# Kernel optimization log

Hardware: AMD Instinct MI355X
Metric: run time of the kernel (lower is better)

Reference implementation:

```python
import jax, jax.numpy as jnp
import numpy as np

HEADS = 4
DIM_HEAD = 32


def setup_inputs() -> dict:
    key = jax.random.key(0)
    k1, k2, k3, k4 = jax.random.split(key, 4)
    dim = 64
    hidden = HEADS * DIM_HEAD  # 128
    x = jax.random.normal(k1, (2, dim, 48, 48, 48), dtype=jnp.float32)
    # 1x1x1 Conv3d weights are just channel-mixing matrices
    w_qkv = jax.random.normal(k2, (3 * hidden, dim), dtype=jnp.float32) * (1.0 / np.sqrt(dim))
    w_out = jax.random.normal(k3, (dim, hidden), dtype=jnp.float32) * (1.0 / np.sqrt(hidden))
    b_out = jax.random.normal(k4, (dim,), dtype=jnp.float32) * 0.01
    return {"x": x, "w_qkv": w_qkv, "w_out": w_out, "b_out": b_out}


def reference(x, w_qkv, w_out, b_out):
    b, c, X, Y, Z = x.shape
    N = X * Y * Z
    xf = x.reshape(b, c, N)  # flatten spatial dims
    # to_qkv: 1x1x1 conv == channel matmul -> [b, 3*H*C, N]
    qkv = jnp.einsum('bci,oc->boi', xf, w_qkv)
    qkv = qkv.reshape(b, 3, HEADS, DIM_HEAD, N)
    q, k, v = qkv[:, 0], qkv[:, 1], qkv[:, 2]  # each [b, h, c, N]
    q = jax.nn.softmax(q, axis=-2)  # softmax over channel dim
    k = jax.nn.softmax(k, axis=-1)  # softmax over spatial dim
    # linear attention: small [c, d] context per head, O(N)
    ctx = jnp.einsum('bhci,bhdi->bhcd', k, v)   # [b, h, c, d]
    out = jnp.einsum('bhcd,bhck->bhdk', ctx, q)  # [b, h, d, N]
    out = out.reshape(b, HEADS * DIM_HEAD, N)
    # combine_heads: 1x1x1 conv with bias
    out = jnp.einsum('bci,oc->boi', out, w_out) + b_out[None, :, None]
    return out.reshape(b, -1, X, Y, Z)
```

## Files before the change

kernel.cpp:

```cpp
#include <hip/hip_runtime.h>
#include <hip/hip_bf16.h>

typedef unsigned int u32;
typedef unsigned short u16;
typedef __attribute__((ext_vector_type(8))) short bf16x8;
typedef __attribute__((ext_vector_type(4))) float f32x4;

#define NPIX 110592
#define NTILES 1728
#define K1_BLOCKS 864
#define K1_TPB 4
#define PART_STRIDE 4224

#define WS_ATB   0
#define WS_P2    8192
#define WS_XPK   75776
#define WS_PART  7153664

union FragU { u32 u[4]; bf16x8 v; };

#define MFMA(a,b,c) __builtin_amdgcn_mfma_f32_16x16x32_bf16((a),(b),(c),0,0,0)

__device__ __forceinline__ void gll16(const float* g, float* l) {
    typedef const __attribute__((address_space(1))) unsigned int* gp_t;
    typedef __attribute__((address_space(3))) unsigned int* lp_t;
    __builtin_amdgcn_global_load_lds((gp_t)g, (lp_t)l, 16, 0, 0);
}
__device__ __forceinline__ u32 pk2(float a, float b) {
    union { __hip_bfloat162 h2; u32 u; } cv;
    cv.h2.x = __float2bfloat16(a);
    cv.h2.y = __float2bfloat16(b);
    return cv.u;
}

__global__ __launch_bounds__(256, 3)
void k1_ctx(const float* __restrict__ x, const float* __restrict__ wq,
            float* __restrict__ ws, int usePart, int R) {
    __shared__ u32 xbh[256 * 32];
    const int blk = blockIdx.x;
    const int p   = threadIdx.x & 63;
    const int og  = __builtin_amdgcn_readfirstlane(threadIdx.x >> 6);
    const int b   = blk / (K1_BLOCKS / 2);
    const int q   = p >> 4;
    const int l15 = p & 15;
    const int yv  = (p & 7) << 2;
    const float* xg = x + (long)b * 64 * NPIX;
    float* part = ws + WS_PART;

    FragU wh[4][2];
    #pragma unroll
    for (int mi = 0; mi < 4; ++mi)
        #pragma unroll
        for (int ks = 0; ks < 2; ++ks) {
            const int kvrow = (mi < 2) ? (og * 32 + mi * 16) : (128 + og * 32 + (mi - 2) * 16);
            const int row = 128 + kvrow + l15;
            const float* wp = wq + row * 64 + ks * 32 + q * 4;
            float4 f0 = *(const float4*)wp;
            float4 f1 = *(const float4*)(wp + 16);
            wh[mi][ks].u[0] = pk2(f0.x, f0.y);
            wh[mi][ks].u[1] = pk2(f0.z, f0.w);
            wh[mi][ks].u[2] = pk2(f1.x, f1.y);
            wh[mi][ks].u[3] = pk2(f1.z, f1.w);
        }

    FragU ones;
    #pragma unroll
    for (int i = 0; i < 4; ++i) ones.u[i] = 0x3F803F80u;

    f32x4 cc[2][2], rsa[2];
    #pragma unroll
    for (int mi = 0; mi < 2; ++mi) {
        #pragma unroll
        for (int ni = 0; ni < 2; ++ni) cc[mi][ni] = (f32x4)0.f;
        rsa[mi] = (f32x4)0.f;
    }

    const long i0g = (long)(blk * K1_TPB - b * NTILES) * 64;
    #pragma unroll
    for (int ch = 0; ch < 2; ++ch) {
        f32x4 xl4[8];
        const float* xr = xg + (long)(og * 16 + ch * 8) * NPIX + i0g + 4 * p;
        #pragma unroll
        for (int i = 0; i < 8; ++i) xl4[i] = *(const f32x4*)(xr + (long)i * NPIX);
        #pragma unroll
        for (int j = 0; j < 4; ++j) {
            const int px = 4 * p + j;
            const int yy = (px & 7) << 2;
            u32 h[4];
            #pragma unroll
            for (int w = 0; w < 4; ++w) h[w] = pk2(xl4[2 * w][j], xl4[2 * w + 1][j]);
            const int sA = (og * 8 + ch * 4) ^ yy;
            *(uint4*)&xbh[px * 32 + sA] = make_uint4(h[0], h[1], h[2], h[3]);
        }
    }
    __syncthreads();

    {
        u32* xpk = (u32*)ws + WS_XPK + (long)blk * 8192;
        #pragma unroll
        for (int i = 0; i < 8; ++i) {
            const int idx = i * 1024 + threadIdx.x * 4;
            uint4 v = *(const uint4*)&xbh[idx];
            *(uint4*)&xpk[idx] = v;
        }
    }

    #pragma unroll 1
    for (int tt = 0; tt < K1_TPB; ++tt) {
        #pragma unroll
        for (int ksp = 0; ksp < 2; ++ksp) {
            f32x4 acc[4][2];
            #pragma unroll
            for (int ni2 = 0; ni2 < 2; ++ni2) {
                const int ni = ksp * 2 + ni2;
                const int rb = (tt * 64 + ni * 16 + l15) * 32;
                FragU bh[2];
                #pragma unroll
                for (int ks = 0; ks < 2; ++ks) {
                    const int c0 = (ks * 16 + 2 * q) ^ yv;
                    const int c1 = (ks * 16 + 2 * q + 8) ^ yv;
                    uint2 t0 = *(const uint2*)&xbh[rb + c0];
                    uint2 t1 = *(const uint2*)&xbh[rb + c1];
                    bh[ks].u[0] = t0.x; bh[ks].u[1] = t0.y;
                    bh[ks].u[2] = t1.x; bh[ks].u[3] = t1.y;
                }
                #pragma unroll
                for (int mi = 0; mi < 4; ++mi) {
                    f32x4 a = (f32x4)0.f;
                    #pragma unroll
                    for (int ks = 0; ks < 2; ++ks)
                        a = MFMA(bh[ks].v, wh[mi][ks].v, a);
                    acc[mi][ni2] = a;
                }
            }
            FragU ak[2], av[2];
            #pragma unroll
            for (int m2 = 0; m2 < 2; ++m2) {
                float e0[4], e1[4];
                #pragma unroll
                for (int j = 0; j < 4; ++j) {
                    e0[j] = __expf(acc[m2][0][j]);
                    e1[j] = __expf(acc[m2][1][j]);
                }
                ak[m2].u[0] = pk2(e0[0], e0[1]);
                ak[m2].u[1] = pk2(e0[2], e0[3]);
                ak[m2].u[2] = pk2(e1[0], e1[1]);
                ak[m2].u[3] = pk2(e1[2], e1[3]);
                av[m2].u[0] = pk2(acc[2 + m2][0][0], acc[2 + m2][0][1]);
                av[m2].u[1] = pk2(acc[2 + m2][0][2], acc[2 + m2][0][3]);
                av[m2].u[2] = pk2(acc[2 + m2][1][0], acc[2 + m2][1][1]);
                av[m2].u[3] = pk2(acc[2 + m2][1][2], acc[2 + m2][1][3]);
            }
            #pragma unroll
            for (int mi = 0; mi < 2; ++mi) {
                #pragma unroll
                for (int nj = 0; nj < 2; ++nj)
                    cc[mi][nj] = MFMA(ak[mi].v, av[nj].v, cc[mi][nj]);
                rsa[mi] = MFMA(ak[mi].v, ones.v, rsa[mi]);
            }
        }
    }

    if (usePart) {
        float* pp = part + (long)blk * PART_STRIDE;
        #pragma unroll
        for (int mi = 0; mi < 2; ++mi)
            #pragma unroll
            for (int ni = 0; ni < 2; ++ni)
                #pragma unroll
                for (int j = 0; j < 4; ++j)
                    pp[og * 1024 + (mi * 16 + q * 4 + j) * 32 + ni * 16 + l15] = cc[mi][ni][j];
        if (l15 == 0) {
            #pragma unroll
            for (int mi = 0; mi < 2; ++mi)
                #pragma unroll
                for (int j = 0; j < 4; ++j)
                    pp[4096 + og * 32 + mi * 16 + q * 4 + j] = rsa[mi][j];
        }
    } else {
        float* pp = part + (long)(b * R + (blk % R)) * PART_STRIDE;
        #pragma unroll
        for (int mi = 0; mi < 2; ++mi)
            #pragma unroll
            for (int ni = 0; ni < 2; ++ni)
                #pragma unroll
                for (int j = 0; j < 4; ++j)
                    atomicAdd(&pp[og * 1024 + (mi * 16 + q * 4 + j) * 32 + ni * 16 + l15], cc[mi][ni][j]);
        if (l15 == 0) {
            #pragma unroll
            for (int mi = 0; mi < 2; ++mi)
                #pragma unroll
                for (int j = 0; j < 4; ++j)
                    atomicAdd(&pp[4096 + og * 32 + mi * 16 + q * 4 + j], rsa[mi][j]);
        }
    }
}

__global__ __launch_bounds__(128)
void k1b_reduce(float* __restrict__ ws, int PB) {
    const int S = 8;
    const int chunk = blockIdx.x % 33;
    const int rem   = blockIdx.x / 33;
    const int b     = rem & 1;
    const int slice = rem >> 1;
    const int j = chunk * 128 + threadIdx.x;
    const int PBh = PB >> 1;
    const float* part = ws + WS_PART;
    float s = 0.f;
    for (int pi = b * PBh + slice; pi < (b + 1) * PBh; pi += S)
        s += part[(long)pi * PART_STRIDE + j];
    ws[WS_P2 + (long)(b * S + slice) * PART_STRIDE + j] = s;
}

__global__ __launch_bounds__(256)
void k2_prepA(const float* __restrict__ wout, float* __restrict__ ws) {
    __shared__ float wo[64 * 129];
    __shared__ float ct[4096];
    __shared__ float rsum[128];
    const int b   = blockIdx.x >> 3;
    const int jb  = blockIdx.x & 7;
    const int tid = threadIdx.x;
    for (int i = tid; i < 8192; i += 256) wo[(i >> 7) * 129 + (i & 127)] = wout[i];
    for (int i = tid; i < 4096; i += 256) {
        float s = 0.f;
        #pragma unroll
        for (int s8 = 0; s8 < 8; ++s8)
            s += ws[WS_P2 + (long)(b * 8 + s8) * PART_STRIDE + i];
        ct[i] = s;
    }
    if (tid < 128) {
        float s = 0.f;
        #pragma unroll
        for (int s8 = 0; s8 < 8; ++s8)
            s += ws[WS_P2 + (long)(b * 8 + s8) * PART_STRIDE + 4096 + tid];
        rsum[tid] = s;
    }
    __syncthreads();
    u32* atb = (u32*)ws + WS_ATB + b * 4096;
    const int o  = tid & 63;
    const int ug = tid >> 6;
    #pragma unroll
    for (int i = 0; i < 2; ++i) {
        const int up = jb * 8 + ug * 2 + i;
        const int hc0 = 2 * up, hc1 = 2 * up + 1;
        const int hh = hc0 >> 5;
        const int c0 = hc0 & 31, c1 = hc1 & 31;
        float s0 = 0.f, s1 = 0.f;
        #pragma unroll
        for (int d = 0; d < 32; ++d) {
            const float w = wo[o * 129 + hh * 32 + d];
            s0 = fmaf(w, ct[hh * 1024 + c0 * 32 + d], s0);
            s1 = fmaf(w, ct[hh * 1024 + c1 * 32 + d], s1);
        }
        atb[up * 64 + o] = pk2(s0 / rsum[hc0], s1 / rsum[hc1]);
    }
}

__global__ __launch_bounds__(256, 3)
void k3_out(const float* __restrict__ x, const float* __restrict__ wq,
            const float* __restrict__ bout, const float* __restrict__ wsf,
            float* __restrict__ out) {
    __shared__ u32 xbh[256 * 32];
    __shared__ u16 qb[64 * 128];
    const int blk = blockIdx.x;
    const int p   = threadIdx.x & 63;
    const int og  = __builtin_amdgcn_readfirstlane(threadIdx.x >> 6);
    const int b   = blk / (K1_BLOCKS / 2);
    const int q   = p >> 4;
    const int l15 = p & 15;
    const int yv  = (p & 7) << 2;
    (void)x;

    {
        const u32* xpk = (const u32*)wsf + WS_XPK + (long)blk * 8192;
        #pragma unroll
        for (int i = 0; i < 8; ++i) {
            const int o32 = og * 2048 + i * 256;
            gll16((const float*)&xpk[o32 + 4 * p], (float*)&xbh[o32]);
        }
    }

    FragU wh[2][2];
    #pragma unroll
    for (int mi = 0; mi < 2; ++mi)
        #pragma unroll
        for (int ks = 0; ks < 2; ++ks) {
            const int row = og * 32 + mi * 16 + l15;
            const float* wp = wq + row * 64 + ks * 32 + q * 4;
            float4 f0 = *(const float4*)wp;
            float4 f1 = *(const float4*)(wp + 16);
            wh[mi][ks].u[0] = pk2(f0.x, f0.y);
            wh[mi][ks].u[1] = pk2(f0.z, f0.w);
            wh[mi][ks].u[2] = pk2(f1.x, f1.y);
            wh[mi][ks].u[3] = pk2(f1.z, f1.w);
        }

    const u32* atb = (const u32*)wsf + WS_ATB + b * 4096;
    FragU af[4];
    #pragma unroll
    for (int ks = 0; ks < 4; ++ks) {
        const int up0 = ks * 16 + 2 * q;
        const int o   = og * 16 + l15;
        af[ks].u[0] = atb[(up0)     * 64 + o];
        af[ks].u[1] = atb[(up0 + 1) * 64 + o];
        af[ks].u[2] = atb[(up0 + 8) * 64 + o];
        af[ks].u[3] = atb[(up0 + 9) * 64 + o];
    }
    const float4 bias = *(const float4*)&bout[og * 16 + q * 4];

    asm volatile("s_waitcnt vmcnt(0)" ::: "memory");
    __syncthreads();

    const long i0g = (long)(blk * K1_TPB - b * NTILES) * 64;
    #pragma unroll 1
    for (int tt = 0; tt < K1_TPB; ++tt) {
        const long i0 = i0g + tt * 64;

        #pragma unroll
        for (int ni = 0; ni < 4; ++ni) {
            const int rb = (tt * 64 + ni * 16 + l15) * 32;
            FragU bh[2];
            #pragma unroll
            for (int ks = 0; ks < 2; ++ks) {
                const int c0 = (ks * 16 + 2 * q) ^ yv;
                const int c1 = (ks * 16 + 2 * q + 8) ^ yv;
                uint2 t0 = *(const uint2*)&xbh[rb + c0];
                uint2 t1 = *(const uint2*)&xbh[rb + c1];
                bh[ks].u[0] = t0.x; bh[ks].u[1] = t0.y;
                bh[ks].u[2] = t1.x; bh[ks].u[3] = t1.y;
            }
            f32x4 a0 = (f32x4)0.f, a1 = (f32x4)0.f;
            #pragma unroll
            for (int ks = 0; ks < 2; ++ks) {
                a0 = MFMA(wh[0][ks].v, bh[ks].v, a0);
                a1 = MFMA(wh[1][ks].v, bh[ks].v, a1);
            }
            float mx = a0[0];
            #pragma unroll
            for (int j = 1; j < 4; ++j) mx = fmaxf(mx, a0[j]);
            #pragma unroll
            for (int j = 0; j < 4; ++j) mx = fmaxf(mx, a1[j]);
            mx = fmaxf(mx, __shfl_xor(mx, 16));
            mx = fmaxf(mx, __shfl_xor(mx, 32));
            float e0[4], e1[4], sm = 0.f;
            #pragma unroll
            for (int j = 0; j < 4; ++j) { e0[j] = __expf(a0[j] - mx); sm += e0[j]; }
            #pragma unroll
            for (int j = 0; j < 4; ++j) { e1[j] = __expf(a1[j] - mx); sm += e1[j]; }
            sm += __shfl_xor(sm, 16);
            sm += __shfl_xor(sm, 32);
            const float inv = 1.0f / sm;
            const int px = ni * 16 + l15;
            const int Xq = (px & 7) << 3;
            u32* qbw = (u32*)qb;
            const int b0 = (px * 128 + ((og * 32 + q * 4) ^ Xq)) >> 1;
            const int b1 = (px * 128 + ((og * 32 + 16 + q * 4) ^ Xq)) >> 1;
            *(uint2*)&qbw[b0] = make_uint2(pk2(e0[0] * inv, e0[1] * inv),
                                           pk2(e0[2] * inv, e0[3] * inv));
            *(uint2*)&qbw[b1] = make_uint2(pk2(e1[0] * inv, e1[1] * inv),
                                           pk2(e1[2] * inv, e1[3] * inv));
        }
        __syncthreads();

        const u32* qb32 = (const u32*)qb;
        #pragma unroll
        for (int ni = 0; ni < 4; ++ni) {
            const int px = ni * 16 + l15;
            const int rb = px * 64;
            f32x4 a3 = (f32x4)0.f;
            #pragma unroll
            for (int ks = 0; ks < 4; ++ks) {
                const int c0 = (ks * 16 + 2 * q) ^ yv;
                const int c1 = (ks * 16 + 2 * q + 8) ^ yv;
                uint2 t0 = *(const uint2*)&qb32[rb + c0];
                uint2 t1 = *(const uint2*)&qb32[rb + c1];
                FragU bq;
                bq.u[0] = t0.x; bq.u[1] = t0.y; bq.u[2] = t1.x; bq.u[3] = t1.y;
                a3 = MFMA(af[ks].v, bq.v, a3);
            }
            #pragma unroll
            for (int j = 0; j < 4; ++j)
                out[((long)b * 64 + og * 16 + q * 4 + j) * NPIX + i0 + px] = a3[j] + bias[j];
        }
        __syncthreads();
    }
}

extern "C" void kernel_launch(void* const* d_in, const int* in_sizes, int n_in,
                              void* d_out, int out_size, void* d_ws, size_t ws_size,
                              hipStream_t stream) {
    (void)in_sizes; (void)n_in; (void)out_size;
    const float* x     = (const float*)d_in[0];
    const float* w_qkv = (const float*)d_in[1];
    const float* w_out = (const float*)d_in[2];
    const float* b_out = (const float*)d_in[3];
    float* out = (float*)d_out;
    float* ws  = (float*)d_ws;

    const size_t need_part = ((size_t)WS_PART + (size_t)K1_BLOCKS * PART_STRIDE) * 4;
    const int usePart = (ws_size >= need_part) ? 1 : 0;
    int R = 8;
    const size_t need_r8 = ((size_t)WS_PART + (size_t)2 * 8 * PART_STRIDE) * 4;
    if (!usePart && ws_size < need_r8) R = 1;
    const int PB = usePart ? K1_BLOCKS : 2 * R;
    float* part = ws + WS_PART;

    if (!usePart)
        hipMemsetAsync(part, 0, (size_t)PB * PART_STRIDE * 4, stream);
    hipLaunchKernelGGL(k1_ctx, dim3(K1_BLOCKS), dim3(256), 0, stream,
                       x, w_qkv, ws, usePart, R);
    hipLaunchKernelGGL(k1b_reduce, dim3(528), dim3(128), 0, stream, ws, PB);
    hipLaunchKernelGGL(k2_prepA, dim3(16), dim3(256), 0, stream, w_out, ws);
    hipLaunchKernelGGL(k3_out, dim3(K1_BLOCKS), dim3(256), 0, stream,
                       x, w_qkv, b_out, ws, out);
}
```

Baseline: 75.26 us.

## Keep per-pixel q softmax in registers and fold bias into projection matrix

The output kernel now has each wave compute all 128 q channels for its own 16 pixels. The softmaxed q fragments feed the output MFMA straight from registers, so the LDS staging buffer and the two block barriers per tile are gone. The bias is folded into the packed A matrix as 0.25*b per entry, which relies on the four per-head channel softmaxes summing to 4. This removes the separate bias add but rounds the bias to bf16. Register use grows (8x2 weight fragments plus 16 A fragments), so launch bounds drop from 3 to 2 blocks per CU.

```diff
diff --git a/kernel.cpp b/kernel.cpp
--- a/kernel.cpp
+++ b/kernel.cpp
@@ -213,7 +213,8 @@
 }
 
 __global__ __launch_bounds__(256)
-void k2_prepA(const float* __restrict__ wout, float* __restrict__ ws) {
+void k2_prepA(const float* __restrict__ wout, const float* __restrict__ bout,
+              float* __restrict__ ws) {
     __shared__ float wo[64 * 129];
     __shared__ float ct[4096];
     __shared__ float rsum[128];
@@ -239,6 +240,7 @@
     u32* atb = (u32*)ws + WS_ATB + b * 4096;
     const int o  = tid & 63;
     const int ug = tid >> 6;
+    const float bo4 = 0.25f * bout[o];
     #pragma unroll
     for (int i = 0; i < 2; ++i) {
         const int up = jb * 8 + ug * 2 + i;
@@ -252,16 +254,15 @@
             s0 = fmaf(w, ct[hh * 1024 + c0 * 32 + d], s0);
             s1 = fmaf(w, ct[hh * 1024 + c1 * 32 + d], s1);
         }
-        atb[up * 64 + o] = pk2(s0 / rsum[hc0], s1 / rsum[hc1]);
-    }
-}
-
-__global__ __launch_bounds__(256, 3)
+        atb[up * 64 + o] = pk2(s0 / rsum[hc0] + bo4, s1 / rsum[hc1] + bo4);
+    }
+}
+
+__global__ __launch_bounds__(256, 2)
 void k3_out(const float* __restrict__ x, const float* __restrict__ wq,
             const float* __restrict__ bout, const float* __restrict__ wsf,
             float* __restrict__ out) {
     __shared__ u32 xbh[256 * 32];
-    __shared__ u16 qb[64 * 128];
     const int blk = blockIdx.x;
     const int p   = threadIdx.x & 63;
     const int og  = __builtin_amdgcn_readfirstlane(threadIdx.x >> 6);
@@ -269,7 +270,7 @@
     const int q   = p >> 4;
     const int l15 = p & 15;
     const int yv  = (p & 7) << 2;
-    (void)x;
+    (void)x; (void)bout;
 
     {
         const u32* xpk = (const u32*)wsf + WS_XPK + (long)blk * 8192;
@@ -280,12 +281,12 @@
         }
     }
 
-    FragU wh[2][2];
-    #pragma unroll
-    for (int mi = 0; mi < 2; ++mi)
+    FragU wh[8][2];
+    #pragma unroll
+    for (int mi = 0; mi < 8; ++mi)
         #pragma unroll
         for (int ks = 0; ks < 2; ++ks) {
-            const int row = og * 32 + mi * 16 + l15;
+            const int row = mi * 16 + l15;
             const float* wp = wq + row * 64 + ks * 32 + q * 4;
             float4 f0 = *(const float4*)wp;
             float4 f1 = *(const float4*)(wp + 16);
@@ -296,17 +297,18 @@
         }
 
     const u32* atb = (const u32*)wsf + WS_ATB + b * 4096;
-    FragU af[4];
-    #pragma unroll
-    for (int ks = 0; ks < 4; ++ks) {
-        const int up0 = ks * 16 + 2 * q;
-        const int o   = og * 16 + l15;
-        af[ks].u[0] = atb[(up0)     * 64 + o];
-        af[ks].u[1] = atb[(up0 + 1) * 64 + o];
-        af[ks].u[2] = atb[(up0 + 8) * 64 + o];
-        af[ks].u[3] = atb[(up0 + 9) * 64 + o];
-    }
-    const float4 bias = *(const float4*)&bout[og * 16 + q * 4];
+    FragU af[4][4];
+    #pragma unroll
+    for (int ob = 0; ob < 4; ++ob)
+        #pragma unroll
+        for (int ks = 0; ks < 4; ++ks) {
+            const int up0 = ks * 16 + 2 * q;
+            const int o   = ob * 16 + l15;
+            af[ob][ks].u[0] = atb[(up0)     * 64 + o];
+            af[ob][ks].u[1] = atb[(up0 + 1) * 64 + o];
+            af[ob][ks].u[2] = atb[(up0 + 8) * 64 + o];
+            af[ob][ks].u[3] = atb[(up0 + 9) * 64 + o];
+        }
 
     asm volatile("s_waitcnt vmcnt(0)" ::: "memory");
     __syncthreads();
@@ -316,10 +318,9 @@
     for (int tt = 0; tt < K1_TPB; ++tt) {
         const long i0 = i0g + tt * 64;
 
-        #pragma unroll
-        for (int ni = 0; ni < 4; ++ni) {
-            const int rb = (tt * 64 + ni * 16 + l15) * 32;
-            FragU bh[2];
+        FragU bh[2];
+        {
+            const int rb = (tt * 64 + og * 16 + l15) * 32;
             #pragma unroll
             for (int ks = 0; ks < 2; ++ks) {
                 const int c0 = (ks * 16 + 2 * q) ^ yv;
@@ -329,60 +330,52 @@
                 bh[ks].u[0] = t0.x; bh[ks].u[1] = t0.y;
                 bh[ks].u[2] = t1.x; bh[ks].u[3] = t1.y;
             }
-            f32x4 a0 = (f32x4)0.f, a1 = (f32x4)0.f;
-            #pragma unroll
-            for (int ks = 0; ks < 2; ++ks) {
-                a0 = MFMA(wh[0][ks].v, bh[ks].v, a0);
-                a1 = MFMA(wh[1][ks].v, bh[ks].v, a1);
-            }
-            float mx = a0[0];
-            #pragma unroll
-            for (int j = 1; j < 4; ++j) mx = fmaxf(mx, a0[j]);
-            #pragma unroll
-            for (int j = 0; j < 4; ++j) mx = fmaxf(mx, a1[j]);
+        }
+        f32x4 acc[8];
+        #pragma unroll
+        for (int mi = 0; mi < 8; ++mi) {
+            f32x4 a = (f32x4)0.f;
+            #pragma unroll
+            for (int ks = 0; ks < 2; ++ks)
+                a = MFMA(wh[mi][ks].v, bh[ks].v, a);
+            acc[mi] = a;
+        }
+
+        FragU bq[4];
+        #pragma unroll
+        for (int h = 0; h < 4; ++h) {
+            float mx = acc[2 * h][0];
+            #pragma unroll
+            for (int j = 1; j < 4; ++j) mx = fmaxf(mx, acc[2 * h][j]);
+            #pragma unroll
+            for (int j = 0; j < 4; ++j) mx = fmaxf(mx, acc[2 * h + 1][j]);
             mx = fmaxf(mx, __shfl_xor(mx, 16));
             mx = fmaxf(mx, __shfl_xor(mx, 32));
             float e0[4], e1[4], sm = 0.f;
             #pragma unroll
-            for (int j = 0; j < 4; ++j) { e0[j] = __expf(a0[j] - mx); sm += e0[j]; }
-            #pragma unroll
-            for (int j = 0; j < 4; ++j) { e1[j] = __expf(a1[j] - mx); sm += e1[j]; }
+            for (int j = 0; j < 4; ++j) { e0[j] = __expf(acc[2 * h][j] - mx); sm += e0[j]; }
+            #pragma unroll
+            for (int j = 0; j < 4; ++j) { e1[j] = __expf(acc[2 * h + 1][j] - mx); sm += e1[j]; }
             sm += __shfl_xor(sm, 16);
             sm += __shfl_xor(sm, 32);
             const float inv = 1.0f / sm;
-            const int px = ni * 16 + l15;
-            const int Xq = (px & 7) << 3;
-            u32* qbw = (u32*)qb;
-            const int b0 = (px * 128 + ((og * 32 + q * 4) ^ Xq)) >> 1;
-            const int b1 = (px * 128 + ((og * 32 + 16 + q * 4) ^ Xq)) >> 1;
-            *(uint2*)&qbw[b0] = make_uint2(pk2(e0[0] * inv, e0[1] * inv),
-                                           pk2(e0[2] * inv, e0[3] * inv));
-            *(uint2*)&qbw[b1] = make_uint2(pk2(e1[0] * inv, e1[1] * inv),
-                                           pk2(e1[2] * inv, e1[3] * inv));
-        }
-        __syncthreads();
-
-        const u32* qb32 = (const u32*)qb;
-        #pragma unroll
-        for (int ni = 0; ni < 4; ++ni) {
-            const int px = ni * 16 + l15;
-            const int rb = px * 64;
+            bq[h].u[0] = pk2(e0[0] * inv, e0[1] * inv);
+            bq[h].u[1] = pk2(e0[2] * inv, e0[3] * inv);
+            bq[h].u[2] = pk2(e1[0] * inv, e1[1] * inv);
+            bq[h].u[3] = pk2(e1[2] * inv, e1[3] * inv);
+        }
+
+        #pragma unroll
+        for (int ob = 0; ob < 4; ++ob) {
             f32x4 a3 = (f32x4)0.f;
             #pragma unroll
-            for (int ks = 0; ks < 4; ++ks) {
-                const int c0 = (ks * 16 + 2 * q) ^ yv;
-                const int c1 = (ks * 16 + 2 * q + 8) ^ yv;
-                uint2 t0 = *(const uint2*)&qb32[rb + c0];
-                uint2 t1 = *(const uint2*)&qb32[rb + c1];
-                FragU bq;
-                bq.u[0] = t0.x; bq.u[1] = t0.y; bq.u[2] = t1.x; bq.u[3] = t1.y;
-                a3 = MFMA(af[ks].v, bq.v, a3);
-            }
+            for (int ks = 0; ks < 4; ++ks)
+                a3 = MFMA(af[ob][ks].v, bq[ks].v, a3);
+            float* op = out + ((long)b * 64 + ob * 16 + q * 4) * NPIX + i0 + og * 16 + l15;
             #pragma unroll
             for (int j = 0; j < 4; ++j)
-                out[((long)b * 64 + og * 16 + q * 4 + j) * NPIX + i0 + px] = a3[j] + bias[j];
-        }
-        __syncthreads();
+                op[(long)j * NPIX] = a3[j];
+        }
     }
 }
 
@@ -410,7 +403,7 @@
     hipLaunchKernelGGL(k1_ctx, dim3(K1_BLOCKS), dim3(256), 0, stream,
                        x, w_qkv, ws, usePart, R);
     hipLaunchKernelGGL(k1b_reduce, dim3(528), dim3(128), 0, stream, ws, PB);
-    hipLaunchKernelGGL(k2_prepA, dim3(16), dim3(256), 0, stream, w_out, ws);
+    hipLaunchKernelGGL(k2_prepA, dim3(16), dim3(256), 0, stream, w_out, b_out, ws);
     hipLaunchKernelGGL(k3_out, dim3(K1_BLOCKS), dim3(256), 0, stream,
                        x, w_qkv, b_out, ws, out);
 }
```

Measured after the change: 81.09 us. 7.7% more time.
